# Kernel tuning notes

Hardware: AMD Instinct MI355X
Metric: run time of the kernel (lower is better)

The kernel has to match this reference:

```python
import jax, jax.numpy as jnp
import numpy as np

BN_EPS = 1e-3


def _knn_group(p1, p2, k):
    # p1, p2: [B, N, 3]. For each point in p1, find k nearest in p2.
    d2 = (jnp.sum(p1 * p1, -1)[:, :, None]
          + jnp.sum(p2 * p2, -1)[:, None, :]
          - 2.0 * jnp.einsum('bnd,bmd->bnm', p1, p2))  # [B,N,N]
    _, idx = jax.lax.top_k(-d2, k)                      # [B,N,k]
    nn = jax.vmap(lambda pts, ind: pts[ind])(p2, idx)   # [B,N,k,3]
    resi = nn - p1[:, :, None, :]                       # [B,N,k,3]
    ss = jnp.sum(resi * resi, -1, keepdims=True)
    dist = jnp.sqrt(jnp.maximum(ss, 1e-12))             # safe norm
    feat = jnp.concatenate([resi, dist], -1)            # [B,N,k,4]
    return feat.transpose(0, 3, 1, 2), nn.transpose(0, 3, 1, 2)  # [B,4,N,k],[B,3,N,k]


def _conv_bn_relu(x, W, b, g, be, m, v):
    # 1x1 conv over channel dim: x [B,C,N,K], W [O,C]
    x = jnp.einsum('bcnk,oc->bonk', x, W) + b[None, :, None, None]
    x = (x - m[None, :, None, None]) * (g / jnp.sqrt(v + BN_EPS))[None, :, None, None] + be[None, :, None, None]
    return jax.nn.relu(x)


def setup_inputs() -> dict:
    key = jax.random.key(0)
    ks = jax.random.split(key, 20)
    B, N = 8, 2048
    chans = [4, 64, 64, 128]
    inp = {
        'points1': jax.random.normal(ks[0], (B, 3, N), jnp.float32),
        'points2': jax.random.normal(ks[1], (B, 3, N), jnp.float32),
    }
    for i in range(3):
        ci, co = chans[i], chans[i + 1]
        base = 2 + i * 6
        scale = 1.0 / np.sqrt(ci)
        inp[f'W{i+1}'] = jax.random.uniform(ks[base], (co, ci), jnp.float32, -scale, scale)
        inp[f'b{i+1}'] = jax.random.uniform(ks[base + 1], (co,), jnp.float32, -scale, scale)
        inp[f'g{i+1}'] = 1.0 + 0.1 * jax.random.normal(ks[base + 2], (co,), jnp.float32)
        inp[f'be{i+1}'] = 0.1 * jax.random.normal(ks[base + 3], (co,), jnp.float32)
        inp[f'm{i+1}'] = 0.05 * jax.random.normal(ks[base + 4], (co,), jnp.float32)
        inp[f'v{i+1}'] = jax.random.uniform(ks[base + 5], (co,), jnp.float32, 0.5, 1.5)
    inp['k'] = 32
    inp['t'] = 1
    return inp


def reference(points1, points2, W1, b1, g1, be1, m1, v1, W2, b2, g2, be2, m2, v2,
              W3, b3, g3, be3, m3, v3, k, t):
    p1 = points1.transpose(0, 2, 1)  # [B,N,3]
    p2 = points2.transpose(0, 2, 1)
    f1, nn1 = _knn_group(p1, p1, k)
    f2, nn2 = _knn_group(p1, p2, k)
    feats = jnp.concatenate([f1, f2], -1)          # [B,4,N,2k]
    grouped = jnp.concatenate([nn1, nn2], -1)      # [B,3,N,2k]
    x = _conv_bn_relu(feats, W1, b1, g1, be1, m1, v1)
    x = _conv_bn_relu(x, W2, b2, g2, be2, m2, v2)
    x = _conv_bn_relu(x, W3, b3, g3, be3, m3, v3)
    x = jnp.max(x, axis=1)                         # [B,N,2k] max over channels
    w = jax.nn.softmax(x, axis=-1)                 # softmax over 2k neighbors
    fused = jnp.sum(w[:, None, :, :] * grouped, -1)  # [B,3,N]
    return fused
```

## Files before the change

kernel.cpp:

```cpp
#include <hip/hip_runtime.h>
#include <hip/hip_bf16.h>
#include <stdint.h>

#define BB 8
#define NN 2048

#define OFF_B1 272
#define OFF_B2 4432
#define OFF_B3 12688
#define IDX_BYTE_OFF 65536
#define T_BASE   (65536 + 2*1024*1024)
#define T1_OFF   T_BASE
#define T2H_OFF  (T1_OFF + 4096)
#define T2L_OFF  (T2H_OFF + 8192)
#define T3H_OFF  (T2L_OFF + 8192)
#define T3L_OFF  (T3H_OFF + 16384)
#define L_T1   0
#define L_T2H  2048
#define L_T2L  6144
#define L_T3H  10240
#define L_T3L  18432
#define L_ELEMS 26624

typedef __attribute__((ext_vector_type(4))) float f32x4;
typedef __attribute__((ext_vector_type(8))) short s16x8;

__device__ __forceinline__ float ldany(const void* p, long i, int isf32) {
    if (isf32) return ((const float*)p)[i];
    uint32_t u = ((uint32_t)((const uint16_t*)p)[i]) << 16;
    float f; __builtin_memcpy(&f, &u, 4); return f;
}
__device__ __forceinline__ uint16_t f2bf(float f) {
    uint32_t u; __builtin_memcpy(&u, &f, 4);
    return (uint16_t)((u + 0x7FFFu + ((u >> 16) & 1u)) >> 16);
}
__device__ __forceinline__ float bf2f(uint16_t h) {
    uint32_t u = ((uint32_t)h) << 16;
    float f; __builtin_memcpy(&f, &u, 4); return f;
}
__device__ __forceinline__ uint32_t pk2(float a, float b) {
    __hip_bfloat162 h = __float22bfloat162_rn(make_float2(a, b));
    uint32_t u; __builtin_memcpy(&u, &h, 4); return u;
}
__device__ __forceinline__ s16x8 mk8(uint32_t a, uint32_t b, uint32_t c, uint32_t d) {
    uint32_t t[4] = {a, b, c, d}; s16x8 r; __builtin_memcpy(&r, t, 16); return r;
}
__device__ __forceinline__ float sane(float v) {
    return (v == v && v > -1e30f && v < 1e30f) ? v : 0.f;
}
__device__ __forceinline__ int mbcnt64(unsigned long long m) {
    return __builtin_amdgcn_mbcnt_hi((uint32_t)(m >> 32),
           __builtin_amdgcn_mbcnt_lo((uint32_t)m, 0));
}
__device__ __forceinline__ int kperm_pos(int kk) {
    int g = kk >> 5, c5 = kk & 31;
    int sub = (c5 >> 4) & 1, q = (c5 >> 2) & 3, r = c5 & 3;
    return 32 * g + 8 * q + 4 * sub + r;
}
__device__ __forceinline__ int fraglin(int o, int p) {
    int g = p >> 5, q = (p >> 3) & 3, e = p & 7;
    return ((((o >> 4) * 2 + g) * 64) + q * 16 + (o & 15)) * 8 + e;
}
__device__ __forceinline__ int fraglin1(int o, int col) {
    int q = col >> 3, e = col & 7;
    return (((o >> 4) * 64) + q * 16 + (o & 15)) * 8 + e;
}

__global__ void kdetect(const void* p1, int* wsi) {
    __shared__ int s_cnt;
    int t = threadIdx.x;
    if (t == 0) s_cnt = 0;
    __syncthreads();
    const uint16_t* u = (const uint16_t*)p1;
    int c = 0;
    for (int i = t; i < 4096; i += 256) {
        uint16_t x = u[i];
        uint32_t e = (x >> 7) & 0xFF;
        c += ((e >= 0x70 && e <= 0x84) || x == 0) ? 1 : 0;
    }
    atomicAdd(&s_cnt, c);
    __syncthreads();
    if (t == 0) wsi[0] = (s_cnt < 3686) ? 1 : 0;
}

__device__ __forceinline__ void do_fold(int gid, int isf32,
                        const void* W1, const void* b1, const void* g1, const void* be1, const void* m1, const void* v1,
                        const void* W2, const void* b2, const void* g2, const void* be2, const void* m2, const void* v2,
                        const void* W3, const void* b3, const void* g3, const void* be3, const void* m3, const void* v3,
                        float* wsf) {
    uint16_t* t1  = (uint16_t*)((char*)wsf + T1_OFF);
    uint16_t* t2h = (uint16_t*)((char*)wsf + T2H_OFF);
    uint16_t* t2l = (uint16_t*)((char*)wsf + T2L_OFF);
    uint16_t* t3h = (uint16_t*)((char*)wsf + T3H_OFF);
    uint16_t* t3l = (uint16_t*)((char*)wsf + T3L_OFF);

    if (gid < 4096) {
        int o = gid >> 6, kk = gid & 63;
        float s = ldany(g2, o, isf32) * rsqrtf(ldany(v2, o, isf32) + 1e-3f);
        float w = ldany(W2, gid, isf32) * s;
        uint16_t wh = f2bf(w);
        int pos = fraglin(o, kperm_pos(kk));
        t2h[pos] = wh; t2l[pos] = f2bf(w - bf2f(wh));
    } else if (gid < 12288) {
        int e = gid - 4096;
        int o = e >> 6, kk = e & 63;
        float s = ldany(g3, o, isf32) * rsqrtf(ldany(v3, o, isf32) + 1e-3f);
        float w = ldany(W3, e, isf32) * s;
        uint16_t wh = f2bf(w);
        int pos = fraglin(o, kperm_pos(kk));
        t3h[pos] = wh; t3l[pos] = f2bf(w - bf2f(wh));
    } else if (gid < 12544) {
        int e = gid - 12288;
        int co = e >> 2, cc = e & 3;
        float s = ldany(g1, co, isf32) * rsqrtf(ldany(v1, co, isf32) + 1e-3f);
        float w = ldany(W1, co*4 + cc, isf32) * s;
        uint16_t wh = f2bf(w), wl = f2bf(w - bf2f(wh));
        t1[fraglin1(co, cc)]     = wh;
        t1[fraglin1(co, 4 + cc)] = wh;
        t1[fraglin1(co, 8 + cc)] = wl;
    } else if (gid < 13824) {
        int e = gid - 12544;
        int co = e / 20, k = e - co * 20;
        t1[fraglin1(co, 12 + k)] = 0;
    } else if (gid < 13888) {
        int o = gid - 13824;
        float s = ldany(g1, o, isf32) * rsqrtf(ldany(v1, o, isf32) + 1e-3f);
        wsf[OFF_B1 + o] = (ldany(b1, o, isf32) - ldany(m1, o, isf32)) * s + ldany(be1, o, isf32);
    } else if (gid < 13952) {
        int o = gid - 13888;
        float s = ldany(g2, o, isf32) * rsqrtf(ldany(v2, o, isf32) + 1e-3f);
        wsf[OFF_B2 + o] = (ldany(b2, o, isf32) - ldany(m2, o, isf32)) * s + ldany(be2, o, isf32);
    } else if (gid < 14080) {
        int o = gid - 13952;
        float s = ldany(g3, o, isf32) * rsqrtf(ldany(v3, o, isf32) + 1e-3f);
        wsf[OFF_B3 + o] = (ldany(b3, o, isf32) - ldany(m3, o, isf32)) * s + ldany(be3, o, isf32);
    }
}

__device__ __forceinline__ void knn_target(const void* p, long base, int isf32, int lane,
                                           float qx, float qy, float qz, float s1,
                                           unsigned long long* sl, uint16_t* dst) {
    uint32_t kb[32];
    if (!isf32) {
        const uint16_t* tpu = (const uint16_t*)p + base;
        const uint4* rx = (const uint4*)(tpu);
        const uint4* ry = (const uint4*)(tpu + NN);
        const uint4* rz = (const uint4*)(tpu + 2*NN);
        #pragma unroll
        for (int i = 0; i < 4; i++) {
            int v4 = i * 64 + lane;
            uint4 X = rx[v4], Y = ry[v4], Z = rz[v4];
            uint32_t xw[4] = {X.x, X.y, X.z, X.w};
            uint32_t yw[4] = {Y.x, Y.y, Y.z, Y.w};
            uint32_t zw[4] = {Z.x, Z.y, Z.z, Z.w};
            #pragma unroll
            for (int j = 0; j < 4; j++) {
                #pragma unroll
                for (int w = 0; w < 2; w++) {
                    uint32_t ux = (w == 0) ? (xw[j] << 16) : (xw[j] & 0xFFFF0000u);
                    uint32_t uy = (w == 0) ? (yw[j] << 16) : (yw[j] & 0xFFFF0000u);
                    uint32_t uz = (w == 0) ? (zw[j] << 16) : (zw[j] & 0xFFFF0000u);
                    float nx, ny, nz;
                    __builtin_memcpy(&nx, &ux, 4); __builtin_memcpy(&ny, &uy, 4); __builtin_memcpy(&nz, &uz, 4);
                    float s2  = nx * nx + ny * ny + nz * nz;
                    float dot = qx * nx + qy * ny + qz * nz;
                    float d2  = fmaxf((s1 + s2) - 2.0f * dot, 0.0f);
                    uint32_t bits; __builtin_memcpy(&bits, &d2, 4);
                    kb[i*8 + j*2 + w] = bits;
                }
            }
        }
    } else {
        const float* tpf = (const float*)p + base;
        #pragma unroll
        for (int i = 0; i < 32; i++) {
            int j = i * 64 + lane;
            float nx = tpf[j];
            float ny = tpf[NN + j];
            float nz = tpf[2*NN + j];
            float s2  = nx * nx + ny * ny + nz * nz;
            float dot = qx * nx + qy * ny + qz * nz;
            float d2  = fmaxf((s1 + s2) - 2.0f * dot, 0.0f);
            uint32_t bits; __builtin_memcpy(&bits, &d2, 4);
            kb[i] = bits;
        }
    }

    uint32_t lo = 0u, hi = 0x7F800001u, tau = 0u;
    uint32_t mid = 0x3E800000u;
    while (true) {
        int c = 0;
        #pragma unroll
        for (int i = 0; i < 32; i++) c += __builtin_popcountll(__ballot(kb[i] < mid));
        if (c >= 32 && c <= 64) { tau = mid; break; }
        if (c < 32) lo = mid; else hi = mid;
        if (hi - lo <= 1u) { tau = hi; break; }
        float mf; __builtin_memcpy(&mf, &mid, 4);
        float nf = mf * __powf(48.0f / (float)(c < 1 ? 1 : c), 0.6666667f);
        uint32_t nm; __builtin_memcpy(&nm, &nf, 4);
        if (!(nm > lo && nm < hi)) nm = lo + ((hi - lo) >> 1);
        mid = nm;
    }

    sl[lane] = ~0ull;
    int basePos = 0;
    #pragma unroll
    for (int i = 0; i < 32; i++) {
        unsigned idxv = isf32 ? (unsigned)(i * 64 + lane)
                              : (unsigned)((i >> 3) * 512 + 8 * lane + (i & 7));
        bool pz = kb[i] < tau;
        unsigned long long m = __ballot(pz);
        int pos = basePos + mbcnt64(m);
        if (pz && pos < 64) sl[pos] = (((unsigned long long)kb[i]) << 32) | idxv;
        basePos += __builtin_popcountll(m);
    }
    unsigned long long key = sl[lane];

    int ns = basePos > 64 ? 64 : basePos;
    unsigned long long mstar = ~0ull;
    if (ns != 32) {
        unsigned long long flo = 0ull;
        unsigned long long fhi = (((unsigned long long)tau) << 32) + 2048ull;
        float tauf; uint32_t tb = tau; __builtin_memcpy(&tauf, &tb, 4);
        float g = tauf * __powf(32.5f / (float)ns, 0.6666667f);
        uint32_t gb; __builtin_memcpy(&gb, &g, 4);
        unsigned long long m0 = ((unsigned long long)gb) << 32;
        if (!(m0 > flo && m0 < fhi)) m0 = flo + ((fhi - flo) >> 1);
        unsigned long long midk = m0;
        while (true) {
            int f = __builtin_popcountll(__ballot(key < midk));
            if (f == 32) { mstar = midk; break; }
            if (f < 32) flo = midk; else fhi = midk;
            if (fhi - flo <= 1ull) { mstar = fhi; break; }
            midk = flo + ((fhi - flo) >> 1);
        }
    }

    bool sel = key < mstar;
    unsigned long long sm = __ballot(sel);
    if (sel) dst[mbcnt64(sm)] = (uint16_t)(key & 0x7FFu);
}

__launch_bounds__(256)
__global__ void k1_knn(const void* p1, const void* p2,
                       const void* W1, const void* b1, const void* g1, const void* be1, const void* m1, const void* v1,
                       const void* W2, const void* b2, const void* g2, const void* be2, const void* m2, const void* v2,
                       const void* W3, const void* b3, const void* g3, const void* be3, const void* m3, const void* v3,
                       float* wsf, const int* wsi, uint16_t* idxout, int isf32arg) {
    __shared__ unsigned long long smem[4 * 64];

    int isf32 = (isf32arg >= 0) ? isf32arg : wsi[0];

    int t = threadIdx.x;
    int lane = threadIdx.x & 63;
    int wave = threadIdx.x >> 6;
    int qidx = blockIdx.x * 4 + wave;
    int b = qidx >> 11, n = qidx & 2047;
    long base = (long)b * 3 * NN;

    float qx = ldany(p1, base + n,        isf32);
    float qy = ldany(p1, base + NN + n,   isf32);
    float qz = ldany(p1, base + 2*NN + n, isf32);
    float s1 = qx * qx + qy * qy + qz * qz;

    unsigned long long* sl = smem + wave * 64;
    long obase = ((long)qidx) << 6;

    knn_target(p1, base, isf32, lane, qx, qy, qz, s1, sl, idxout + obase);

    __builtin_amdgcn_sched_barrier(0);
    asm volatile("" ::: "memory");

    knn_target(p2, base, isf32, lane, qx, qy, qz, s1, sl, idxout + obase + 32);

    if (blockIdx.x < 55) {
        int gid = blockIdx.x * 256 + t;
        do_fold(gid, isf32,
                W1, b1, g1, be1, m1, v1,
                W2, b2, g2, be2, m2, v2,
                W3, b3, g3, be3, m3, v3, wsf);
    }
}

__launch_bounds__(512, 2)
__global__ void k2_mlp(const void* p1, const void* p2, const float* __restrict__ wsf, const int* wsi,
                       const uint16_t* __restrict__ idxin, void* outp, int isf32arg) {
    __shared__ uint4 shw4[L_ELEMS / 8];

    {
        const uint4* src = (const uint4*)((const char*)wsf + T1_OFF);
        for (int i = threadIdx.x; i < L_ELEMS / 8; i += 512) shw4[i] = src[i];
    }
    __syncthreads();
    const uint16_t* shw = (const uint16_t*)shw4;
    const uint16_t* T1  = shw + L_T1;
    const uint16_t* T2H = shw + L_T2H;
    const uint16_t* T2L = shw + L_T2L;
    const uint16_t* T3H = shw + L_T3H;
    const uint16_t* T3L = shw + L_T3L;

    int isf32 = (isf32arg >= 0) ? isf32arg : wsi[0];
    int lane = threadIdx.x & 63;
    int wave = threadIdx.x >> 6;
    int c = lane & 15;
    int q = lane >> 4;
    int qidx = blockIdx.x * 8 + wave;
    int b = qidx >> 11, n = qidx & 2047;
    long base = (long)b * 3 * NN;

    float qx = sane(ldany(p1, base + n,        isf32));
    float qy = sane(ldany(p1, base + NN + n,   isf32));
    float qz = sane(ldany(p1, base + 2*NN + n, isf32));

    int idx = idxin[((long)qidx << 6) + lane] & 2047;
    const void* sp = (lane < 32) ? p1 : p2;
    float nx = sane(ldany(sp, base + idx,        isf32));
    float ny = sane(ldany(sp, base + NN + idx,   isf32));
    float nz = sane(ldany(sp, base + 2*NN + idx, isf32));

    float r0 = nx - qx, r1 = ny - qy, r2 = nz - qz;
    float ss = fmaf(r0, r0, fmaf(r1, r1, r2 * r2));
    float dist = sqrtf(fmaxf(ss, 1e-12f));

    const float* B1 = wsf + OFF_B1;
    const float* B2 = wsf + OFF_B2;
    const float* B3 = wsf + OFF_B3;

    auto mkfrag = [](const f32x4& dlo, const f32x4& dhi) -> s16x8 {
        return mk8(pk2(fmaxf(dlo[0], 0.f), fmaxf(dlo[1], 0.f)),
                   pk2(fmaxf(dlo[2], 0.f), fmaxf(dlo[3], 0.f)),
                   pk2(fmaxf(dhi[0], 0.f), fmaxf(dhi[1], 0.f)),
                   pk2(fmaxf(dhi[2], 0.f), fmaxf(dhi[3], 0.f)));
    };

    s16x8 b1f[4];
    #pragma unroll
    for (int nt = 0; nt < 4; nt++) {
        int src = 16 * nt + c;
        float f0 = __shfl(r0, src, 64);
        float f1 = __shfl(r1, src, 64);
        float f2v = __shfl(r2, src, 64);
        float f3v = __shfl(dist, src, 64);
        uint16_t h0 = f2bf(f0), h1 = f2bf(f1), h2 = f2bf(f2v), h3 = f2bf(f3v);
        uint16_t l0 = f2bf(f0 - bf2f(h0)), l1 = f2bf(f1 - bf2f(h1));
        uint16_t l2 = f2bf(f2v - bf2f(h2)), l3 = f2bf(f3v - bf2f(h3));
        s16x8 v;
        bool qa = (q < 2);
        bool qb = (q == 0);
        v[0] = qa ? (short)h0 : (short)0;
        v[1] = qa ? (short)h1 : (short)0;
        v[2] = qa ? (short)h2 : (short)0;
        v[3] = qa ? (short)h3 : (short)0;
        v[4] = qb ? (short)l0 : (short)0;
        v[5] = qb ? (short)l1 : (short)0;
        v[6] = qb ? (short)l2 : (short)0;
        v[7] = qb ? (short)l3 : (short)0;
        b1f[nt] = v;
    }

    s16x8 fh[2][4];
    {
        f32x4 d1[4][4];
        #pragma unroll
        for (int mt = 0; mt < 4; mt++) {
            s16x8 a1 = *(const s16x8*)(T1 + (mt * 64 + lane) * 8);
            f32x4 bias = *(const f32x4*)(B1 + 16 * mt + 4 * q);
            #pragma unroll
            for (int nt = 0; nt < 4; nt++) {
                d1[mt][nt] = __builtin_amdgcn_mfma_f32_16x16x32_bf16(a1, b1f[nt], bias, 0, 0, 0);
            }
        }
        #pragma unroll
        for (int g = 0; g < 2; g++)
            #pragma unroll
            for (int nt = 0; nt < 4; nt++) fh[g][nt] = mkfrag(d1[2*g][nt], d1[2*g+1][nt]);
    }

    s16x8 f3h[2][4];
    {
        f32x4 d2[4][4];
        #pragma unroll
        for (int mt = 0; mt < 4; mt++) {
            f32x4 bias = *(const f32x4*)(B2 + 16 * mt + 4 * q);
            #pragma unroll
            for (int nt = 0; nt < 4; nt++) d2[mt][nt] = bias;
        }
        #pragma unroll
        for (int g = 0; g < 2; g++) {
            #pragma unroll
            for (int mt = 0; mt < 4; mt++) {
                s16x8 ah = *(const s16x8*)(T2H + ((mt * 2 + g) * 64 + lane) * 8);
                s16x8 al = *(const s16x8*)(T2L + ((mt * 2 + g) * 64 + lane) * 8);
                #pragma unroll
                for (int nt = 0; nt < 4; nt++) {
                    f32x4 acc = d2[mt][nt];
                    acc = __builtin_amdgcn_mfma_f32_16x16x32_bf16(ah, fh[g][nt], acc, 0, 0, 0);
                    acc = __builtin_amdgcn_mfma_f32_16x16x32_bf16(al, fh[g][nt], acc, 0, 0, 0);
                    d2[mt][nt] = acc;
                }
            }
        }
        #pragma unroll
        for (int g = 0; g < 2; g++)
            #pragma unroll
            for (int nt = 0; nt < 4; nt++) f3h[g][nt] = mkfrag(d2[2*g][nt], d2[2*g+1][nt]);
    }

    float mx[4] = {-1e30f, -1e30f, -1e30f, -1e30f};
    #pragma unroll
    for (int mt = 0; mt < 8; mt++) {
        f32x4 bias = *(const f32x4*)(B3 + 16 * mt + 4 * q);
        f32x4 acc[4];
        #pragma unroll
        for (int nt = 0; nt < 4; nt++) acc[nt] = bias;
        #pragma unroll
        for (int g = 0; g < 2; g++) {
            s16x8 ah = *(const s16x8*)(T3H + ((mt * 2 + g) * 64 + lane) * 8);
            s16x8 al = *(const s16x8*)(T3L + ((mt * 2 + g) * 64 + lane) * 8);
            #pragma unroll
            for (int nt = 0; nt < 4; nt++) {
                f32x4 a = acc[nt];
                a = __builtin_amdgcn_mfma_f32_16x16x32_bf16(ah, f3h[g][nt], a, 0, 0, 0);
                a = __builtin_amdgcn_mfma_f32_16x16x32_bf16(al, f3h[g][nt], a, 0, 0, 0);
                acc[nt] = a;
            }
        }
        #pragma unroll
        for (int nt = 0; nt < 4; nt++) {
            mx[nt] = fmaxf(mx[nt], fmaxf(fmaxf(acc[nt][0], acc[nt][1]), fmaxf(acc[nt][2], acc[nt][3])));
        }
    }

    #pragma unroll
    for (int nt = 0; nt < 4; nt++) {
        mx[nt] = fmaxf(mx[nt], __shfl_xor(mx[nt], 16, 64));
        mx[nt] = fmaxf(mx[nt], __shfl_xor(mx[nt], 32, 64));
        mx[nt] = fmaxf(mx[nt], 0.f);
    }
    float mall = fmaxf(fmaxf(mx[0], mx[1]), fmaxf(mx[2], mx[3]));
    #pragma unroll
    for (int m = 1; m < 16; m <<= 1) mall = fmaxf(mall, __shfl_xor(mall, m, 64));
    float e0 = __expf(mx[0] - mall), e1 = __expf(mx[1] - mall);
    float e2 = __expf(mx[2] - mall), e3 = __expf(mx[3] - mall);
    float s = e0 + e1 + e2 + e3;
    #pragma unroll
    for (int m = 1; m < 16; m <<= 1) s += __shfl_xor(s, m, 64);
    float eown = (q == 0) ? e0 : (q == 1) ? e1 : (q == 2) ? e2 : e3;
    float w = eown / s;

    float sx = w * nx, sy = w * ny, sz = w * nz;
    #pragma unroll
    for (int m = 1; m < 64; m <<= 1) {
        sx += __shfl_xor(sx, m, 64);
        sy += __shfl_xor(sy, m, 64);
        sz += __shfl_xor(sz, m, 64);
    }

    if (lane < 3) {
        float v = (lane == 0) ? sx : ((lane == 1) ? sy : sz);
        long oi = base + (long)lane * NN + n;
        if (isf32) {
            ((float*)outp)[oi] = v;
        } else {
            ((uint16_t*)outp)[oi] = f2bf(v);
        }
    }
}

extern "C" void kernel_launch(void* const* d_in, const int* in_sizes, int n_in,
                              void* d_out, int out_size, void* d_ws, size_t ws_size,
                              hipStream_t stream) {
    const void* p1 = d_in[0];
    const void* p2 = d_in[1];
    float* wsf = (float*)d_ws;
    int*   wsi = (int*)d_ws;
    uint16_t* idxbuf = (uint16_t*)((char*)d_ws + IDX_BYTE_OFF);

    int isf32 = -1;
    if (in_sizes && n_in >= 1) {
        if (in_sizes[0] == BB * 3 * NN * 4)      isf32 = 1;
        else if (in_sizes[0] == BB * 3 * NN * 2) isf32 = 0;
    }
    if (isf32 < 0) {
        kdetect<<<1, 256, 0, stream>>>(p1, wsi);
    }

    k1_knn<<<(BB * NN) / 4, 256, 0, stream>>>(p1, p2,
        d_in[2],  d_in[3],  d_in[4],  d_in[5],  d_in[6],  d_in[7],
        d_in[8],  d_in[9],  d_in[10], d_in[11], d_in[12], d_in[13],
        d_in[14], d_in[15], d_in[16], d_in[17], d_in[18], d_in[19],
        wsf, wsi, idxbuf, isf32);

    k2_mlp<<<(BB * NN) / 8, 512, 0, stream>>>(p1, p2, wsf, wsi, idxbuf, d_out, isf32);
}
```

Baseline: 244.5 us.

## Fuse kNN selection and MLP into one kernel, split weight folding out

Moves the BN weight folding into a small separate kernel and fuses the kNN selection with the MLP/softmax stage. Neighbor indices now stay in shared memory instead of going through a global index buffer, and one kernel launch is removed. In exchange the MLP reads the folded weights directly from global memory rather than staging them in LDS. It also changes from 512-thread blocks with launch bounds (512,2) to 256-thread blocks, so the heavy kNN register usage now shares occupancy with the MFMA stage.

```diff
diff --git a/kernel.cpp b/kernel.cpp
--- a/kernel.cpp
+++ b/kernel.cpp
@@ -8,19 +8,12 @@
 #define OFF_B1 272
 #define OFF_B2 4432
 #define OFF_B3 12688
-#define IDX_BYTE_OFF 65536
 #define T_BASE   (65536 + 2*1024*1024)
 #define T1_OFF   T_BASE
 #define T2H_OFF  (T1_OFF + 4096)
 #define T2L_OFF  (T2H_OFF + 8192)
 #define T3H_OFF  (T2L_OFF + 8192)
 #define T3L_OFF  (T3H_OFF + 16384)
-#define L_T1   0
-#define L_T2H  2048
-#define L_T2L  6144
-#define L_T3H  10240
-#define L_T3L  18432
-#define L_ELEMS 26624
 
 typedef __attribute__((ext_vector_type(4))) float f32x4;
 typedef __attribute__((ext_vector_type(8))) short s16x8;
@@ -83,11 +76,13 @@
     if (t == 0) wsi[0] = (s_cnt < 3686) ? 1 : 0;
 }
 
-__device__ __forceinline__ void do_fold(int gid, int isf32,
-                        const void* W1, const void* b1, const void* g1, const void* be1, const void* m1, const void* v1,
+__global__ void k0_fold(const void* W1, const void* b1, const void* g1, const void* be1, const void* m1, const void* v1,
                         const void* W2, const void* b2, const void* g2, const void* be2, const void* m2, const void* v2,
                         const void* W3, const void* b3, const void* g3, const void* be3, const void* m3, const void* v3,
-                        float* wsf) {
+                        float* wsf, const int* wsi, int isf32arg) {
+    int isf32 = (isf32arg >= 0) ? isf32arg : wsi[0];
+    int gid = blockIdx.x * 256 + threadIdx.x;
+
     uint16_t* t1  = (uint16_t*)((char*)wsf + T1_OFF);
     uint16_t* t2h = (uint16_t*)((char*)wsf + T2H_OFF);
     uint16_t* t2l = (uint16_t*)((char*)wsf + T2L_OFF);
@@ -242,16 +237,12 @@
 }
 
 __launch_bounds__(256)
-__global__ void k1_knn(const void* p1, const void* p2,
-                       const void* W1, const void* b1, const void* g1, const void* be1, const void* m1, const void* v1,
-                       const void* W2, const void* b2, const void* g2, const void* be2, const void* m2, const void* v2,
-                       const void* W3, const void* b3, const void* g3, const void* be3, const void* m3, const void* v3,
-                       float* wsf, const int* wsi, uint16_t* idxout, int isf32arg) {
+__global__ void kfused(const void* p1, const void* p2, const float* __restrict__ wsf, const int* wsi,
+                       void* outp, int isf32arg) {
     __shared__ unsigned long long smem[4 * 64];
+    __shared__ uint16_t sidx[4 * 64];
 
     int isf32 = (isf32arg >= 0) ? isf32arg : wsi[0];
-
-    int t = threadIdx.x;
     int lane = threadIdx.x & 63;
     int wave = threadIdx.x >> 6;
     int qidx = blockIdx.x * 4 + wave;
@@ -264,67 +255,41 @@
     float s1 = qx * qx + qy * qy + qz * qz;
 
     unsigned long long* sl = smem + wave * 64;
-    long obase = ((long)qidx) << 6;
-
-    knn_target(p1, base, isf32, lane, qx, qy, qz, s1, sl, idxout + obase);
+    uint16_t* si = sidx + wave * 64;
+
+    knn_target(p1, base, isf32, lane, qx, qy, qz, s1, sl, si);
 
     __builtin_amdgcn_sched_barrier(0);
     asm volatile("" ::: "memory");
 
-    knn_target(p2, base, isf32, lane, qx, qy, qz, s1, sl, idxout + obase + 32);
-
-    if (blockIdx.x < 55) {
-        int gid = blockIdx.x * 256 + t;
-        do_fold(gid, isf32,
-                W1, b1, g1, be1, m1, v1,
-                W2, b2, g2, be2, m2, v2,
-                W3, b3, g3, be3, m3, v3, wsf);
-    }
-}
-
-__launch_bounds__(512, 2)
-__global__ void k2_mlp(const void* p1, const void* p2, const float* __restrict__ wsf, const int* wsi,
-                       const uint16_t* __restrict__ idxin, void* outp, int isf32arg) {
-    __shared__ uint4 shw4[L_ELEMS / 8];
-
-    {
-        const uint4* src = (const uint4*)((const char*)wsf + T1_OFF);
-        for (int i = threadIdx.x; i < L_ELEMS / 8; i += 512) shw4[i] = src[i];
-    }
-    __syncthreads();
-    const uint16_t* shw = (const uint16_t*)shw4;
-    const uint16_t* T1  = shw + L_T1;
-    const uint16_t* T2H = shw + L_T2H;
-    const uint16_t* T2L = shw + L_T2L;
-    const uint16_t* T3H = shw + L_T3H;
-    const uint16_t* T3L = shw + L_T3L;
-
-    int isf32 = (isf32arg >= 0) ? isf32arg : wsi[0];
-    int lane = threadIdx.x & 63;
-    int wave = threadIdx.x >> 6;
+    knn_target(p2, base, isf32, lane, qx, qy, qz, s1, sl, si + 32);
+
+    __builtin_amdgcn_sched_barrier(0);
+    asm volatile("" ::: "memory");
+
     int c = lane & 15;
     int q = lane >> 4;
-    int qidx = blockIdx.x * 8 + wave;
-    int b = qidx >> 11, n = qidx & 2047;
-    long base = (long)b * 3 * NN;
-
-    float qx = sane(ldany(p1, base + n,        isf32));
-    float qy = sane(ldany(p1, base + NN + n,   isf32));
-    float qz = sane(ldany(p1, base + 2*NN + n, isf32));
-
-    int idx = idxin[((long)qidx << 6) + lane] & 2047;
+
+    const uint16_t* T1  = (const uint16_t*)((const char*)wsf + T1_OFF);
+    const uint16_t* T2H = (const uint16_t*)((const char*)wsf + T2H_OFF);
+    const uint16_t* T2L = (const uint16_t*)((const char*)wsf + T2L_OFF);
+    const uint16_t* T3H = (const uint16_t*)((const char*)wsf + T3H_OFF);
+    const uint16_t* T3L = (const uint16_t*)((const char*)wsf + T3L_OFF);
+    const float* B1 = wsf + OFF_B1;
+    const float* B2 = wsf + OFF_B2;
+    const float* B3 = wsf + OFF_B3;
+
+    float qsx = sane(qx), qsy = sane(qy), qsz = sane(qz);
+
+    int idx = si[lane] & 2047;
     const void* sp = (lane < 32) ? p1 : p2;
     float nx = sane(ldany(sp, base + idx,        isf32));
     float ny = sane(ldany(sp, base + NN + idx,   isf32));
     float nz = sane(ldany(sp, base + 2*NN + idx, isf32));
 
-    float r0 = nx - qx, r1 = ny - qy, r2 = nz - qz;
+    float r0 = nx - qsx, r1 = ny - qsy, r2 = nz - qsz;
     float ss = fmaf(r0, r0, fmaf(r1, r1, r2 * r2));
     float dist = sqrtf(fmaxf(ss, 1e-12f));
-
-    const float* B1 = wsf + OFF_B1;
-    const float* B2 = wsf + OFF_B2;
-    const float* B3 = wsf + OFF_B3;
 
     auto mkfrag = [](const f32x4& dlo, const f32x4& dhi) -> s16x8 {
         return mk8(pk2(fmaxf(dlo[0], 0.f), fmaxf(dlo[1], 0.f)),
@@ -474,7 +439,6 @@
     const void* p2 = d_in[1];
     float* wsf = (float*)d_ws;
     int*   wsi = (int*)d_ws;
-    uint16_t* idxbuf = (uint16_t*)((char*)d_ws + IDX_BYTE_OFF);
 
     int isf32 = -1;
     if (in_sizes && n_in >= 1) {
@@ -485,11 +449,11 @@
         kdetect<<<1, 256, 0, stream>>>(p1, wsi);
     }
 
-    k1_knn<<<(BB * NN) / 4, 256, 0, stream>>>(p1, p2,
+    k0_fold<<<55, 256, 0, stream>>>(
         d_in[2],  d_in[3],  d_in[4],  d_in[5],  d_in[6],  d_in[7],
         d_in[8],  d_in[9],  d_in[10], d_in[11], d_in[12], d_in[13],
         d_in[14], d_in[15], d_in[16], d_in[17], d_in[18], d_in[19],
-        wsf, wsi, idxbuf, isf32);
-
-    k2_mlp<<<(BB * NN) / 8, 512, 0, stream>>>(p1, p2, wsf, wsi, idxbuf, d_out, isf32);
-}
+        wsf, wsi, isf32);
+
+    kfused<<<(BB * NN) / 4, 256, 0, stream>>>(p1, p2, wsf, wsi, d_out, isf32);
+}
```

Result: slower. 328.5 us (+34.4%).

## Precompute packed xyz plus squared norm into workspace for KNN and MLP

Applied to the files above, without the earlier changes.

Adds a small pre-kernel that converts both point clouds from planar layout (bf16 or fp32) into an interleaved float4 of x,y,z and |p|^2 in the workspace. The KNN kernel then does one 16-byte load per candidate and skips recomputing each candidate's norm and the bf16 unpacking. The MLP kernel gathers neighbours with one vector load instead of three scattered ones. The cost is an extra launch plus more memory traffic when the inputs are bf16, since the packed form is twice the size.

```diff
diff --git a/kernel.cpp b/kernel.cpp
--- a/kernel.cpp
+++ b/kernel.cpp
@@ -15,6 +15,7 @@
 #define T2L_OFF  (T2H_OFF + 8192)
 #define T3H_OFF  (T2L_OFF + 8192)
 #define T3L_OFF  (T3H_OFF + 16384)
+#define XYZ_OFF  2228224
 #define L_T1   0
 #define L_T2H  2048
 #define L_T2L  6144
@@ -81,6 +82,22 @@
     atomicAdd(&s_cnt, c);
     __syncthreads();
     if (t == 0) wsi[0] = (s_cnt < 3686) ? 1 : 0;
+}
+
+__global__ void k0_xyz(const void* p1, const void* p2, float* wsf, const int* wsi, int isf32arg) {
+    int isf32 = (isf32arg >= 0) ? isf32arg : wsi[0];
+    int gid = blockIdx.x * 256 + threadIdx.x;
+    int tgt = gid >> 14, rem = gid & 16383;
+    int b = rem >> 11, n = rem & 2047;
+    const void* pp = tgt ? p2 : p1;
+    long bb = (long)b * 3 * NN;
+    float x = ldany(pp, bb + n,        isf32);
+    float y = ldany(pp, bb + NN + n,   isf32);
+    float z = ldany(pp, bb + 2*NN + n, isf32);
+    f32x4 v;
+    v[0] = x; v[1] = y; v[2] = z;
+    v[3] = x * x + y * y + z * z;
+    ((f32x4*)((char*)wsf + XYZ_OFF))[gid] = v;
 }
 
 __device__ __forceinline__ void do_fold(int gid, int isf32,
@@ -137,53 +154,17 @@
     }
 }
 
-__device__ __forceinline__ void knn_target(const void* p, long base, int isf32, int lane,
+__device__ __forceinline__ void knn_target(const f32x4* __restrict__ tb, int lane,
                                            float qx, float qy, float qz, float s1,
                                            unsigned long long* sl, uint16_t* dst) {
     uint32_t kb[32];
-    if (!isf32) {
-        const uint16_t* tpu = (const uint16_t*)p + base;
-        const uint4* rx = (const uint4*)(tpu);
-        const uint4* ry = (const uint4*)(tpu + NN);
-        const uint4* rz = (const uint4*)(tpu + 2*NN);
-        #pragma unroll
-        for (int i = 0; i < 4; i++) {
-            int v4 = i * 64 + lane;
-            uint4 X = rx[v4], Y = ry[v4], Z = rz[v4];
-            uint32_t xw[4] = {X.x, X.y, X.z, X.w};
-            uint32_t yw[4] = {Y.x, Y.y, Y.z, Y.w};
-            uint32_t zw[4] = {Z.x, Z.y, Z.z, Z.w};
-            #pragma unroll
-            for (int j = 0; j < 4; j++) {
-                #pragma unroll
-                for (int w = 0; w < 2; w++) {
-                    uint32_t ux = (w == 0) ? (xw[j] << 16) : (xw[j] & 0xFFFF0000u);
-                    uint32_t uy = (w == 0) ? (yw[j] << 16) : (yw[j] & 0xFFFF0000u);
-                    uint32_t uz = (w == 0) ? (zw[j] << 16) : (zw[j] & 0xFFFF0000u);
-                    float nx, ny, nz;
-                    __builtin_memcpy(&nx, &ux, 4); __builtin_memcpy(&ny, &uy, 4); __builtin_memcpy(&nz, &uz, 4);
-                    float s2  = nx * nx + ny * ny + nz * nz;
-                    float dot = qx * nx + qy * ny + qz * nz;
-                    float d2  = fmaxf((s1 + s2) - 2.0f * dot, 0.0f);
-                    uint32_t bits; __builtin_memcpy(&bits, &d2, 4);
-                    kb[i*8 + j*2 + w] = bits;
-                }
-            }
-        }
-    } else {
-        const float* tpf = (const float*)p + base;
-        #pragma unroll
-        for (int i = 0; i < 32; i++) {
-            int j = i * 64 + lane;
-            float nx = tpf[j];
-            float ny = tpf[NN + j];
-            float nz = tpf[2*NN + j];
-            float s2  = nx * nx + ny * ny + nz * nz;
-            float dot = qx * nx + qy * ny + qz * nz;
-            float d2  = fmaxf((s1 + s2) - 2.0f * dot, 0.0f);
-            uint32_t bits; __builtin_memcpy(&bits, &d2, 4);
-            kb[i] = bits;
-        }
+    #pragma unroll
+    for (int i = 0; i < 32; i++) {
+        f32x4 P = tb[i * 64 + lane];
+        float dot = qx * P[0] + qy * P[1] + qz * P[2];
+        float d2  = fmaxf((s1 + P[3]) - 2.0f * dot, 0.0f);
+        uint32_t bits; __builtin_memcpy(&bits, &d2, 4);
+        kb[i] = bits;
     }
 
     uint32_t lo = 0u, hi = 0x7F800001u, tau = 0u;
@@ -206,8 +187,7 @@
     int basePos = 0;
     #pragma unroll
     for (int i = 0; i < 32; i++) {
-        unsigned idxv = isf32 ? (unsigned)(i * 64 + lane)
-                              : (unsigned)((i >> 3) * 512 + 8 * lane + (i & 7));
+        unsigned idxv = (unsigned)(i * 64 + lane);
         bool pz = kb[i] < tau;
         unsigned long long m = __ballot(pz);
         int pos = basePos + mbcnt64(m);
@@ -221,7 +201,7 @@
     if (ns != 32) {
         unsigned long long flo = 0ull;
         unsigned long long fhi = (((unsigned long long)tau) << 32) + 2048ull;
-        float tauf; uint32_t tb = tau; __builtin_memcpy(&tauf, &tb, 4);
+        float tauf; uint32_t tb2 = tau; __builtin_memcpy(&tauf, &tb2, 4);
         float g = tauf * __powf(32.5f / (float)ns, 0.6666667f);
         uint32_t gb; __builtin_memcpy(&gb, &g, 4);
         unsigned long long m0 = ((unsigned long long)gb) << 32;
@@ -242,7 +222,7 @@
 }
 
 __launch_bounds__(256)
-__global__ void k1_knn(const void* p1, const void* p2,
+__global__ void k1_knn(const float* __restrict__ wsf_ro,
                        const void* W1, const void* b1, const void* g1, const void* be1, const void* m1, const void* v1,
                        const void* W2, const void* b2, const void* g2, const void* be2, const void* m2, const void* v2,
                        const void* W3, const void* b3, const void* g3, const void* be3, const void* m3, const void* v3,
@@ -256,22 +236,23 @@
     int wave = threadIdx.x >> 6;
     int qidx = blockIdx.x * 4 + wave;
     int b = qidx >> 11, n = qidx & 2047;
-    long base = (long)b * 3 * NN;
-
-    float qx = ldany(p1, base + n,        isf32);
-    float qy = ldany(p1, base + NN + n,   isf32);
-    float qz = ldany(p1, base + 2*NN + n, isf32);
-    float s1 = qx * qx + qy * qy + qz * qz;
+
+    const f32x4* xyz = (const f32x4*)((const char*)wsf_ro + XYZ_OFF);
+    const f32x4* tb1 = xyz + (long)b * NN;
+    const f32x4* tb2 = xyz + (long)(8 + b) * NN;
+
+    f32x4 Q = tb1[n];
+    float qx = Q[0], qy = Q[1], qz = Q[2], s1 = Q[3];
 
     unsigned long long* sl = smem + wave * 64;
     long obase = ((long)qidx) << 6;
 
-    knn_target(p1, base, isf32, lane, qx, qy, qz, s1, sl, idxout + obase);
+    knn_target(tb1, lane, qx, qy, qz, s1, sl, idxout + obase);
 
     __builtin_amdgcn_sched_barrier(0);
     asm volatile("" ::: "memory");
 
-    knn_target(p2, base, isf32, lane, qx, qy, qz, s1, sl, idxout + obase + 32);
+    knn_target(tb2, lane, qx, qy, qz, s1, sl, idxout + obase + 32);
 
     if (blockIdx.x < 55) {
         int gid = blockIdx.x * 256 + t;
@@ -283,7 +264,7 @@
 }
 
 __launch_bounds__(512, 2)
-__global__ void k2_mlp(const void* p1, const void* p2, const float* __restrict__ wsf, const int* wsi,
+__global__ void k2_mlp(const float* __restrict__ wsf, const int* wsi,
                        const uint16_t* __restrict__ idxin, void* outp, int isf32arg) {
     __shared__ uint4 shw4[L_ELEMS / 8];
 
@@ -308,15 +289,15 @@
     int b = qidx >> 11, n = qidx & 2047;
     long base = (long)b * 3 * NN;
 
-    float qx = sane(ldany(p1, base + n,        isf32));
-    float qy = sane(ldany(p1, base + NN + n,   isf32));
-    float qz = sane(ldany(p1, base + 2*NN + n, isf32));
+    const f32x4* xyz = (const f32x4*)((const char*)wsf + XYZ_OFF);
+
+    f32x4 Q = xyz[(long)b * NN + n];
+    float qx = sane(Q[0]), qy = sane(Q[1]), qz = sane(Q[2]);
 
     int idx = idxin[((long)qidx << 6) + lane] & 2047;
-    const void* sp = (lane < 32) ? p1 : p2;
-    float nx = sane(ldany(sp, base + idx,        isf32));
-    float ny = sane(ldany(sp, base + NN + idx,   isf32));
-    float nz = sane(ldany(sp, base + 2*NN + idx, isf32));
+    int tgt = (lane < 32) ? 0 : 1;
+    f32x4 P = xyz[(long)(tgt * 8 + b) * NN + idx];
+    float nx = sane(P[0]), ny = sane(P[1]), nz = sane(P[2]);
 
     float r0 = nx - qx, r1 = ny - qy, r2 = nz - qz;
     float ss = fmaf(r0, r0, fmaf(r1, r1, r2 * r2));
@@ -485,11 +466,13 @@
         kdetect<<<1, 256, 0, stream>>>(p1, wsi);
     }
 
-    k1_knn<<<(BB * NN) / 4, 256, 0, stream>>>(p1, p2,
+    k0_xyz<<<128, 256, 0, stream>>>(p1, p2, wsf, wsi, isf32);
+
+    k1_knn<<<(BB * NN) / 4, 256, 0, stream>>>(wsf,
         d_in[2],  d_in[3],  d_in[4],  d_in[5],  d_in[6],  d_in[7],
         d_in[8],  d_in[9],  d_in[10], d_in[11], d_in[12], d_in[13],
         d_in[14], d_in[15], d_in[16], d_in[17], d_in[18], d_in[19],
         wsf, wsi, idxbuf, isf32);
 
-    k2_mlp<<<(BB * NN) / 8, 512, 0, stream>>>(p1, p2, wsf, wsi, idxbuf, d_out, isf32);
-}
+    k2_mlp<<<(BB * NN) / 8, 512, 0, stream>>>(wsf, wsi, idxbuf, d_out, isf32);
+}
```

Result: faster. 226.7 us (median of 2 runs) (-7.3%).
